# Performance work log

Measured on AMD Instinct MI355X. Metric: run time of the kernel, lower is better.

## Reference

```python
import jax, jax.numpy as jnp
import numpy as np

B, S, D, H = 2, 2048, 1024, 16
HD = D // H


def setup_inputs() -> dict:
    key = jax.random.key(0)
    ks = jax.random.split(key, 9)
    x = jax.random.normal(ks[0], (B, S, D), dtype=jnp.float32)
    scale = 1.0 / np.sqrt(D)
    Wq = jax.random.normal(ks[1], (D, D), dtype=jnp.float32) * scale
    bq = jnp.zeros((D,), dtype=jnp.float32)
    Wk = jax.random.normal(ks[2], (D, D), dtype=jnp.float32) * scale
    bk = jnp.zeros((D,), dtype=jnp.float32)
    Wv = jax.random.normal(ks[3], (D, D), dtype=jnp.float32) * scale
    bv = jnp.zeros((D,), dtype=jnp.float32)
    Wo = jax.random.normal(ks[4], (D, D), dtype=jnp.float32) * scale
    bo = jnp.zeros((D,), dtype=jnp.float32)
    return {"x": x, "Wq": Wq, "bq": bq, "Wk": Wk, "bk": bk,
            "Wv": Wv, "bv": bv, "Wo": Wo, "bo": bo}


def reference(x, Wq, bq, Wk, bk, Wv, bv, Wo, bo):
    b, s, d = x.shape
    h, hd = H, HD
    # torch Linear: y = x @ W.T + b
    q = (x @ Wq.T + bq).reshape(b, s, h, hd).transpose(0, 2, 1, 3)  # (b,h,s,hd)
    k = (x @ Wk.T + bk).reshape(b, s, h, hd).transpose(0, 2, 1, 3)
    v = (x @ Wv.T + bv).reshape(b, s, h, hd).transpose(0, 2, 1, 3)
    scores = jnp.einsum('bhqd,bhkd->bhqk', q, k) / np.sqrt(hd)  # (b,h,s,s)
    # FAITHFUL to source: softmax over dim=1 (head axis), not the key axis.
    attn = jax.nn.softmax(scores, axis=1)
    # dropout is identity at inference
    out = jnp.einsum('bhqk,bhkd->bhqd', attn, v)  # (b,h,s,hd)
    out = out.transpose(0, 2, 1, 3).reshape(b, s, d)
    return out @ Wo.T + bo
```

## Files before the change

kernel.cpp:

```cpp
#include <hip/hip_runtime.h>
#include <hip/hip_bf16.h>
#include <cstdint>
#include <cstddef>


typedef __bf16 bf16x8 __attribute__((ext_vector_type(8)));
typedef __bf16 bf16x4 __attribute__((ext_vector_type(4)));
typedef float floatx4 __attribute__((ext_vector_type(4)));

#define S_LEN 2048
#define DIM 1024
#define NH 16
#define HD 64
#define MTOT 4096

__global__ void cast_f32_bf16(const float* __restrict__ s, __bf16* __restrict__ d, int n) {
    int i = (blockIdx.x * blockDim.x + threadIdx.x) * 4;
    if (i < n) {
        float4 v = *(const float4*)&s[i];
        bf16x4 o;
        o.x = (__bf16)v.x; o.y = (__bf16)v.y; o.z = (__bf16)v.z; o.w = (__bf16)v.w;
        *(bf16x4*)&d[i] = o;
    }
}

template <typename OUT_T>
__global__ __launch_bounds__(256, 2) void gemm_bt(const __bf16* __restrict__ A,
                                                  const __bf16* __restrict__ Bw,
                                                  const float* __restrict__ bias,
                                                  OUT_T* __restrict__ C,
                                                  int M, int N, int K) {
    const int tm = blockIdx.y * 128;
    const int tn = blockIdx.x * 128;
    __shared__ __bf16 As[128 * 40];
    __shared__ __bf16 Bs[128 * 40];
    const int tid = threadIdx.x;
    const int wid = tid >> 6, lane = tid & 63;
    const int wm = (wid >> 1) * 64, wn = (wid & 1) * 64;
    const int l15 = lane & 15, quad = lane >> 4;
    floatx4 acc[4][4] = {};
    for (int k0 = 0; k0 < K; k0 += 32) {
        __syncthreads();
#pragma unroll
        for (int i = 0; i < 2; ++i) {
            int c = i * 256 + tid;
            int row = c >> 2, kc = (c & 3) * 8;
            *(bf16x8*)&As[row * 40 + kc] = *(const bf16x8*)&A[(size_t)(tm + row) * K + k0 + kc];
            *(bf16x8*)&Bs[row * 40 + kc] = *(const bf16x8*)&Bw[(size_t)(tn + row) * K + k0 + kc];
        }
        __syncthreads();
        bf16x8 af[4], bf[4];
#pragma unroll
        for (int t = 0; t < 4; ++t) {
            af[t] = *(const bf16x8*)&As[(wm + t * 16 + l15) * 40 + quad * 8];
            bf[t] = *(const bf16x8*)&Bs[(wn + t * 16 + l15) * 40 + quad * 8];
        }
#pragma unroll
        for (int im = 0; im < 4; ++im)
#pragma unroll
            for (int in = 0; in < 4; ++in)
                acc[im][in] = __builtin_amdgcn_mfma_f32_16x16x32_bf16(af[im], bf[in], acc[im][in], 0, 0, 0);
    }
#pragma unroll
    for (int im = 0; im < 4; ++im)
#pragma unroll
        for (int in = 0; in < 4; ++in)
#pragma unroll
            for (int r = 0; r < 4; ++r) {
                int row = tm + wm + im * 16 + quad * 4 + r;
                int col = tn + wn + in * 16 + l15;
                float v = acc[im][in][r] + bias[col];
                C[(size_t)row * N + col] = (OUT_T)v;
            }
}

__global__ void transpose_bf16(const __bf16* __restrict__ src, __bf16* __restrict__ dst,
                               int M, int N) {
    __shared__ __bf16 t[32][33];
    int bx = blockIdx.x * 32;
    int by = blockIdx.y * 32;
    int x = threadIdx.x, y = threadIdx.y;
#pragma unroll
    for (int i = 0; i < 32; i += 8) t[y + i][x] = src[(size_t)(by + y + i) * N + bx + x];
    __syncthreads();
#pragma unroll
    for (int i = 0; i < 32; i += 8) dst[(size_t)(bx + y + i) * M + by + x] = t[x][y + i];
}

__global__ __launch_bounds__(256, 2) void den_kernel(const __bf16* __restrict__ Q,
                                                     const __bf16* __restrict__ Km,
                                                     __bf16* __restrict__ rd) {
    const int b = blockIdx.z, qt = blockIdx.y * 128, kt = blockIdx.x * 128;
    __shared__ __bf16 Qs[128 * 72];
    __shared__ __bf16 Ks[128 * 72];
    const int tid = threadIdx.x;
    const int wid = tid >> 6, lane = tid & 63;
    const int wm = (wid >> 1) * 64, wn = (wid & 1) * 64;
    const int l15 = lane & 15, quad = lane >> 4;
    float den[4][4][4] = {};
    const size_t qbase = ((size_t)b * S_LEN + qt) * DIM;
    const size_t kbase = ((size_t)b * S_LEN + kt) * DIM;
    for (int h = 0; h < NH; ++h) {
        __syncthreads();
#pragma unroll
        for (int i = 0; i < 4; ++i) {
            int c = i * 256 + tid;
            int row = c >> 3, kc = (c & 7) * 8;
            *(bf16x8*)&Qs[row * 72 + kc] = *(const bf16x8*)&Q[qbase + (size_t)row * DIM + h * HD + kc];
            *(bf16x8*)&Ks[row * 72 + kc] = *(const bf16x8*)&Km[kbase + (size_t)row * DIM + h * HD + kc];
        }
        __syncthreads();
        floatx4 acc[4][4] = {};
#pragma unroll
        for (int kc = 0; kc < 2; ++kc) {
            bf16x8 af[4], bf[4];
#pragma unroll
            for (int t = 0; t < 4; ++t) {
                af[t] = *(const bf16x8*)&Qs[(wm + t * 16 + l15) * 72 + kc * 32 + quad * 8];
                bf[t] = *(const bf16x8*)&Ks[(wn + t * 16 + l15) * 72 + kc * 32 + quad * 8];
            }
#pragma unroll
            for (int im = 0; im < 4; ++im)
#pragma unroll
                for (int in = 0; in < 4; ++in)
                    acc[im][in] = __builtin_amdgcn_mfma_f32_16x16x32_bf16(af[im], bf[in], acc[im][in], 0, 0, 0);
        }
#pragma unroll
        for (int im = 0; im < 4; ++im)
#pragma unroll
            for (int in = 0; in < 4; ++in)
#pragma unroll
                for (int r = 0; r < 4; ++r)
                    den[im][in][r] += __expf(acc[im][in][r] * 0.125f);
    }
#pragma unroll
    for (int im = 0; im < 4; ++im)
#pragma unroll
        for (int in = 0; in < 4; ++in)
#pragma unroll
            for (int r = 0; r < 4; ++r) {
                int row = qt + wm + im * 16 + quad * 4 + r;
                int col = kt + wn + in * 16 + l15;
                rd[((size_t)b * S_LEN + row) * S_LEN + col] = (__bf16)(1.0f / den[im][in][r]);
            }
}

__global__ __launch_bounds__(256, 2) void attn_kernel(const __bf16* __restrict__ Q,
                                                      const __bf16* __restrict__ Km,
                                                      const __bf16* __restrict__ Vt,
                                                      const __bf16* __restrict__ rd,
                                                      __bf16* __restrict__ AO) {
    const int qt = blockIdx.x * 128, h = blockIdx.y, b = blockIdx.z;
    __shared__ __bf16 KV[128 * 72];
    __shared__ __bf16 Ps[128 * 136];
    const int tid = threadIdx.x;
    const int wid = tid >> 6, lane = tid & 63;
    const int wm = (wid >> 1) * 64, wn = (wid & 1) * 64;
    const int l15 = lane & 15, quad = lane >> 4;
    const size_t qrow0 = (size_t)b * S_LEN + qt;
    bf16x8 qf[4][2];
#pragma unroll
    for (int im = 0; im < 4; ++im)
#pragma unroll
        for (int kc = 0; kc < 2; ++kc)
            qf[im][kc] = *(const bf16x8*)&Q[(qrow0 + wm + im * 16 + l15) * DIM + h * HD + kc * 32 + quad * 8];
    floatx4 oacc[2][4] = {};
    const size_t kbase = ((size_t)b * S_LEN) * DIM;
    for (int kt = 0; kt < S_LEN; kt += 128) {
        __syncthreads();
#pragma unroll
        for (int i = 0; i < 4; ++i) {
            int c = i * 256 + tid;
            int row = c >> 3, kc = (c & 7) * 8;
            *(bf16x8*)&KV[row * 72 + kc] = *(const bf16x8*)&Km[kbase + (size_t)(kt + row) * DIM + h * HD + kc];
        }
#pragma unroll
        for (int i = 0; i < 8; ++i) {
            int c = i * 256 + tid;
            int row = c >> 4, cc = (c & 15) * 8;
            *(bf16x8*)&Ps[row * 136 + cc] =
                *(const bf16x8*)&rd[((size_t)b * S_LEN + qt + row) * S_LEN + kt + cc];
        }
        __syncthreads();
        floatx4 acc[4][4] = {};
#pragma unroll
        for (int kc = 0; kc < 2; ++kc) {
            bf16x8 bfr[4];
#pragma unroll
            for (int t = 0; t < 4; ++t)
                bfr[t] = *(const bf16x8*)&KV[(wn + t * 16 + l15) * 72 + kc * 32 + quad * 8];
#pragma unroll
            for (int im = 0; im < 4; ++im)
#pragma unroll
                for (int in = 0; in < 4; ++in)
                    acc[im][in] = __builtin_amdgcn_mfma_f32_16x16x32_bf16(qf[im][kc], bfr[in], acc[im][in], 0, 0, 0);
        }
#pragma unroll
        for (int im = 0; im < 4; ++im)
#pragma unroll
            for (int in = 0; in < 4; ++in)
#pragma unroll
                for (int r = 0; r < 4; ++r) {
                    int row = wm + im * 16 + quad * 4 + r;
                    int col = wn + in * 16 + l15;
                    float rdv = (float)Ps[row * 136 + col];
                    float p = __expf(acc[im][in][r] * 0.125f) * rdv;
                    Ps[row * 136 + col] = (__bf16)p;
                }
        __syncthreads();
#pragma unroll
        for (int i = 0; i < 4; ++i) {
            int c = i * 256 + tid;
            int row = c >> 4, cc = (c & 15) * 8;
            *(bf16x8*)&KV[row * 136 + cc] =
                *(const bf16x8*)&Vt[((size_t)h * HD + row) * MTOT + b * S_LEN + kt + cc];
        }
        __syncthreads();
        const int qr = wid * 32;
#pragma unroll
        for (int kc = 0; kc < 4; ++kc) {
            bf16x8 pa[2], vb[4];
#pragma unroll
            for (int t = 0; t < 2; ++t)
                pa[t] = *(const bf16x8*)&Ps[(qr + t * 16 + l15) * 136 + kc * 32 + quad * 8];
#pragma unroll
            for (int t = 0; t < 4; ++t)
                vb[t] = *(const bf16x8*)&KV[(t * 16 + l15) * 136 + kc * 32 + quad * 8];
#pragma unroll
            for (int im = 0; im < 2; ++im)
#pragma unroll
                for (int n = 0; n < 4; ++n)
                    oacc[im][n] = __builtin_amdgcn_mfma_f32_16x16x32_bf16(pa[im], vb[n], oacc[im][n], 0, 0, 0);
        }
    }
    const int qr = wid * 32;
#pragma unroll
    for (int im = 0; im < 2; ++im)
#pragma unroll
        for (int n = 0; n < 4; ++n)
#pragma unroll
            for (int r = 0; r < 4; ++r) {
                int row = qt + qr + im * 16 + quad * 4 + r;
                int col = h * HD + n * 16 + l15;
                AO[((size_t)b * S_LEN + row) * DIM + col] = (__bf16)(oacc[im][n][r]);
            }
}

extern "C" void kernel_launch(void* const* d_in, const int* in_sizes, int n_in,
                              void* d_out, int out_size, void* d_ws, size_t ws_size,
                              hipStream_t stream) {
    const float* x  = (const float*)d_in[0];
    const float* Wq = (const float*)d_in[1];
    const float* bq = (const float*)d_in[2];
    const float* Wk = (const float*)d_in[3];
    const float* bk = (const float*)d_in[4];
    const float* Wv = (const float*)d_in[5];
    const float* bv = (const float*)d_in[6];
    const float* Wo = (const float*)d_in[7];
    const float* bo = (const float*)d_in[8];
    float* out = (float*)d_out;

    char* ws = (char*)d_ws;
    const size_t MB = 1u << 20;
    __bf16* xb  = (__bf16*)(ws);
    __bf16* Wqb = (__bf16*)(ws + 8 * MB);
    __bf16* Wkb = (__bf16*)(ws + 10 * MB);
    __bf16* Wvb = (__bf16*)(ws + 12 * MB);
    __bf16* Wob = (__bf16*)(ws + 14 * MB);
    __bf16* Qb  = (__bf16*)(ws + 16 * MB);
    __bf16* Kb  = (__bf16*)(ws + 24 * MB);
    __bf16* Vb  = (__bf16*)(ws + 32 * MB);
    __bf16* Vtb = (__bf16*)(ws + 40 * MB);
    __bf16* rd  = (__bf16*)(ws + 48 * MB);
    __bf16* AOb = (__bf16*)(ws + 64 * MB);

    cast_f32_bf16<<<4096, 256, 0, stream>>>(x,  xb,  MTOT * DIM);
    cast_f32_bf16<<<1024, 256, 0, stream>>>(Wq, Wqb, DIM * DIM);
    cast_f32_bf16<<<1024, 256, 0, stream>>>(Wk, Wkb, DIM * DIM);
    cast_f32_bf16<<<1024, 256, 0, stream>>>(Wv, Wvb, DIM * DIM);
    cast_f32_bf16<<<1024, 256, 0, stream>>>(Wo, Wob, DIM * DIM);

    dim3 gproj(DIM / 128, MTOT / 128);
    gemm_bt<__bf16><<<gproj, 256, 0, stream>>>(xb, Wqb, bq, Qb, MTOT, DIM, DIM);
    gemm_bt<__bf16><<<gproj, 256, 0, stream>>>(xb, Wkb, bk, Kb, MTOT, DIM, DIM);
    gemm_bt<__bf16><<<gproj, 256, 0, stream>>>(xb, Wvb, bv, Vb, MTOT, DIM, DIM);

    dim3 gtr(DIM / 32, MTOT / 32);
    transpose_bf16<<<gtr, dim3(32, 8), 0, stream>>>(Vb, Vtb, MTOT, DIM);

    dim3 gden(S_LEN / 128, S_LEN / 128, 2);
    den_kernel<<<gden, 256, 0, stream>>>(Qb, Kb, rd);

    dim3 gattn(S_LEN / 128, NH, 2);
    attn_kernel<<<gattn, 256, 0, stream>>>(Qb, Kb, Vtb, rd, AOb);

    gemm_bt<float><<<gproj, 256, 0, stream>>>(AOb, Wob, bo, out, MTOT, DIM, DIM);
}
```

Before: 317.1 us.

## Rewrite GEMM, denominator and attention kernels with direct global-to-LDS loads

```diff
diff --git a/kernel.cpp b/kernel.cpp
--- a/kernel.cpp
+++ b/kernel.cpp
@@ -6,6 +6,8 @@
 
 typedef __bf16 bf16x8 __attribute__((ext_vector_type(8)));
 typedef __bf16 bf16x4 __attribute__((ext_vector_type(4)));
+typedef _Float16 f16x4 __attribute__((ext_vector_type(4)));
+typedef _Float16 f16x8 __attribute__((ext_vector_type(8)));
 typedef float floatx4 __attribute__((ext_vector_type(4)));
 
 #define S_LEN 2048
@@ -13,6 +15,12 @@
 #define NH 16
 #define HD 64
 #define MTOT 4096
+
+__device__ __forceinline__ void g2l16(const void* g, void* l) {
+    __builtin_amdgcn_global_load_lds(
+        (const __attribute__((address_space(1))) void*)g,
+        (__attribute__((address_space(3))) void*)l, 16, 0, 0);
+}
 
 __global__ void cast_f32_bf16(const float* __restrict__ s, __bf16* __restrict__ d, int n) {
     int i = (blockIdx.x * blockDim.x + threadIdx.x) * 4;
@@ -25,60 +33,65 @@
 }
 
 template <typename OUT_T>
-__global__ __launch_bounds__(256, 2) void gemm_bt(const __bf16* __restrict__ A,
-                                                  const __bf16* __restrict__ Bw,
-                                                  const float* __restrict__ bias,
-                                                  OUT_T* __restrict__ C,
-                                                  int M, int N, int K) {
-    const int tm = blockIdx.y * 128;
-    const int tn = blockIdx.x * 128;
-    __shared__ __bf16 As[128 * 40];
-    __shared__ __bf16 Bs[128 * 40];
-    const int tid = threadIdx.x;
-    const int wid = tid >> 6, lane = tid & 63;
-    const int wm = (wid >> 1) * 64, wn = (wid & 1) * 64;
+__global__ __launch_bounds__(256, 2) void gemm_bt2(const __bf16* __restrict__ A,
+                                                   const __bf16* __restrict__ Bw,
+                                                   const float* __restrict__ bias,
+                                                   OUT_T* __restrict__ C,
+                                                   int M, int N, int K) {
+    const int tm = blockIdx.y * 128, tn = blockIdx.x * 64;
+    __shared__ __bf16 As[2 * 128 * 32];
+    __shared__ __bf16 Bs[2 * 64 * 32];
+    const int tid = threadIdx.x, wid = tid >> 6, lane = tid & 63;
     const int l15 = lane & 15, quad = lane >> 4;
-    floatx4 acc[4][4] = {};
-    for (int k0 = 0; k0 < K; k0 += 32) {
-        __syncthreads();
+    const int wm = (wid >> 1) * 64, wn = (wid & 1) * 32;
+    floatx4 acc[4][2] = {};
+    for (int k0 = 0; k0 < K; k0 += 64) {
+        __syncthreads();
+#pragma unroll
+        for (int i = 0; i < 4; ++i) {
+            int slot = i * 256 + tid;
+            int p = slot >> 9, r = (slot >> 2) & 127, c8 = (slot & 3) * 8;
+            g2l16(&A[(size_t)(tm + r) * K + k0 + p * 32 + c8], &As[slot * 8]);
+        }
 #pragma unroll
         for (int i = 0; i < 2; ++i) {
-            int c = i * 256 + tid;
-            int row = c >> 2, kc = (c & 3) * 8;
-            *(bf16x8*)&As[row * 40 + kc] = *(const bf16x8*)&A[(size_t)(tm + row) * K + k0 + kc];
-            *(bf16x8*)&Bs[row * 40 + kc] = *(const bf16x8*)&Bw[(size_t)(tn + row) * K + k0 + kc];
-        }
-        __syncthreads();
-        bf16x8 af[4], bf[4];
-#pragma unroll
-        for (int t = 0; t < 4; ++t) {
-            af[t] = *(const bf16x8*)&As[(wm + t * 16 + l15) * 40 + quad * 8];
-            bf[t] = *(const bf16x8*)&Bs[(wn + t * 16 + l15) * 40 + quad * 8];
-        }
-#pragma unroll
-        for (int im = 0; im < 4; ++im)
-#pragma unroll
-            for (int in = 0; in < 4; ++in)
-                acc[im][in] = __builtin_amdgcn_mfma_f32_16x16x32_bf16(af[im], bf[in], acc[im][in], 0, 0, 0);
+            int slot = i * 256 + tid;
+            int p = slot >> 8, r = (slot >> 2) & 63, c8 = (slot & 3) * 8;
+            g2l16(&Bw[(size_t)(tn + r) * K + k0 + p * 32 + c8], &Bs[slot * 8]);
+        }
+        __syncthreads();
+#pragma unroll
+        for (int kc = 0; kc < 2; ++kc) {
+            bf16x8 af[4], bf[2];
+#pragma unroll
+            for (int t = 0; t < 4; ++t)
+                af[t] = *(const bf16x8*)&As[kc * 4096 + (wm + t * 16 + l15) * 32 + quad * 8];
+#pragma unroll
+            for (int t = 0; t < 2; ++t)
+                bf[t] = *(const bf16x8*)&Bs[kc * 2048 + (wn + t * 16 + l15) * 32 + quad * 8];
+#pragma unroll
+            for (int im = 0; im < 4; ++im)
+#pragma unroll
+                for (int in = 0; in < 2; ++in)
+                    acc[im][in] = __builtin_amdgcn_mfma_f32_16x16x32_bf16(af[im], bf[in], acc[im][in], 0, 0, 0);
+        }
     }
 #pragma unroll
     for (int im = 0; im < 4; ++im)
 #pragma unroll
-        for (int in = 0; in < 4; ++in)
+        for (int in = 0; in < 2; ++in)
 #pragma unroll
             for (int r = 0; r < 4; ++r) {
                 int row = tm + wm + im * 16 + quad * 4 + r;
                 int col = tn + wn + in * 16 + l15;
-                float v = acc[im][in][r] + bias[col];
-                C[(size_t)row * N + col] = (OUT_T)v;
-            }
-}
-
-__global__ void transpose_bf16(const __bf16* __restrict__ src, __bf16* __restrict__ dst,
-                               int M, int N) {
-    __shared__ __bf16 t[32][33];
-    int bx = blockIdx.x * 32;
-    int by = blockIdx.y * 32;
+                C[(size_t)row * N + col] = (OUT_T)(acc[im][in][r] + bias[col]);
+            }
+}
+
+__global__ void transpose16(const ushort* __restrict__ src, ushort* __restrict__ dst,
+                            int M, int N) {
+    __shared__ ushort t[32][33];
+    int bx = blockIdx.x * 32, by = blockIdx.y * 32;
     int x = threadIdx.x, y = threadIdx.y;
 #pragma unroll
     for (int i = 0; i < 32; i += 8) t[y + i][x] = src[(size_t)(by + y + i) * N + bx + x];
@@ -87,162 +100,131 @@
     for (int i = 0; i < 32; i += 8) dst[(size_t)(bx + y + i) * M + by + x] = t[x][y + i];
 }
 
-__global__ __launch_bounds__(256, 2) void den_kernel(const __bf16* __restrict__ Q,
-                                                     const __bf16* __restrict__ Km,
-                                                     __bf16* __restrict__ rd) {
-    const int b = blockIdx.z, qt = blockIdx.y * 128, kt = blockIdx.x * 128;
-    __shared__ __bf16 Qs[128 * 72];
-    __shared__ __bf16 Ks[128 * 72];
-    const int tid = threadIdx.x;
-    const int wid = tid >> 6, lane = tid & 63;
-    const int wm = (wid >> 1) * 64, wn = (wid & 1) * 64;
+__global__ __launch_bounds__(256, 4) void den2(const __bf16* __restrict__ Q,
+                                               const __bf16* __restrict__ Km,
+                                               __bf16* __restrict__ rd) {
+    const int kt = blockIdx.x * 128, qt = blockIdx.y * 64, b = blockIdx.z;
+    __shared__ __bf16 Qs[2 * 64 * 32];
+    __shared__ __bf16 Ks[2 * 128 * 32];
+    const int tid = threadIdx.x, wid = tid >> 6, lane = tid & 63;
     const int l15 = lane & 15, quad = lane >> 4;
-    float den[4][4][4] = {};
-    const size_t qbase = ((size_t)b * S_LEN + qt) * DIM;
-    const size_t kbase = ((size_t)b * S_LEN + kt) * DIM;
+    const int wq = wid * 16;
+    floatx4 dsum[8] = {};
     for (int h = 0; h < NH; ++h) {
         __syncthreads();
 #pragma unroll
-        for (int i = 0; i < 4; ++i) {
-            int c = i * 256 + tid;
-            int row = c >> 3, kc = (c & 7) * 8;
-            *(bf16x8*)&Qs[row * 72 + kc] = *(const bf16x8*)&Q[qbase + (size_t)row * DIM + h * HD + kc];
-            *(bf16x8*)&Ks[row * 72 + kc] = *(const bf16x8*)&Km[kbase + (size_t)row * DIM + h * HD + kc];
-        }
-        __syncthreads();
-        floatx4 acc[4][4] = {};
-#pragma unroll
-        for (int kc = 0; kc < 2; ++kc) {
-            bf16x8 af[4], bf[4];
-#pragma unroll
-            for (int t = 0; t < 4; ++t) {
-                af[t] = *(const bf16x8*)&Qs[(wm + t * 16 + l15) * 72 + kc * 32 + quad * 8];
-                bf[t] = *(const bf16x8*)&Ks[(wn + t * 16 + l15) * 72 + kc * 32 + quad * 8];
-            }
-#pragma unroll
-            for (int im = 0; im < 4; ++im)
-#pragma unroll
-                for (int in = 0; in < 4; ++in)
-                    acc[im][in] = __builtin_amdgcn_mfma_f32_16x16x32_bf16(af[im], bf[in], acc[im][in], 0, 0, 0);
-        }
-#pragma unroll
-        for (int im = 0; im < 4; ++im)
-#pragma unroll
-            for (int in = 0; in < 4; ++in)
-#pragma unroll
-                for (int r = 0; r < 4; ++r)
-                    den[im][in][r] += __expf(acc[im][in][r] * 0.125f);
-    }
-#pragma unroll
-    for (int im = 0; im < 4; ++im)
-#pragma unroll
-        for (int in = 0; in < 4; ++in)
+        for (int i = 0; i < 2; ++i) {
+            int slot = i * 256 + tid;
+            int p = slot >> 8, r = (slot >> 2) & 63, c8 = (slot & 3) * 8;
+            g2l16(&Q[(size_t)(b * S_LEN + qt + r) * DIM + h * HD + p * 32 + c8], &Qs[slot * 8]);
+        }
+#pragma unroll
+        for (int i = 0; i < 4; ++i) {
+            int slot = i * 256 + tid;
+            int p = slot >> 9, r = (slot >> 2) & 127, c8 = (slot & 3) * 8;
+            g2l16(&Km[(size_t)(b * S_LEN + kt + r) * DIM + h * HD + p * 32 + c8], &Ks[slot * 8]);
+        }
+        __syncthreads();
+        bf16x8 af0 = *(const bf16x8*)&Qs[(wq + l15) * 32 + quad * 8];
+        bf16x8 af1 = *(const bf16x8*)&Qs[2048 + (wq + l15) * 32 + quad * 8];
+#pragma unroll
+        for (int n = 0; n < 8; ++n) {
+            bf16x8 b0 = *(const bf16x8*)&Ks[(n * 16 + l15) * 32 + quad * 8];
+            bf16x8 b1 = *(const bf16x8*)&Ks[4096 + (n * 16 + l15) * 32 + quad * 8];
+            floatx4 acc = {};
+            acc = __builtin_amdgcn_mfma_f32_16x16x32_bf16(af0, b0, acc, 0, 0, 0);
+            acc = __builtin_amdgcn_mfma_f32_16x16x32_bf16(af1, b1, acc, 0, 0, 0);
+#pragma unroll
+            for (int r = 0; r < 4; ++r) dsum[n][r] += __expf(acc[r] * 0.125f);
+        }
+    }
+#pragma unroll
+    for (int n = 0; n < 8; ++n)
+#pragma unroll
+        for (int r = 0; r < 4; ++r) {
+            int q = qt + wq + quad * 4 + r;
+            int k = kt + n * 16 + l15;
+            rd[(size_t)(b * S_LEN + q) * S_LEN + k] = (__bf16)(1.0f / dsum[n][r]);
+        }
+}
+
+__global__ __launch_bounds__(256, 2) void attn2(const __bf16* __restrict__ Q,
+                                                const __bf16* __restrict__ Km,
+                                                const _Float16* __restrict__ Vt,
+                                                const __bf16* __restrict__ rd,
+                                                __bf16* __restrict__ AO) {
+    const int qt = blockIdx.x * 128, h = blockIdx.y, b = blockIdx.z;
+    __shared__ __bf16 Ks[2 * 128 * 32];
+    __shared__ __bf16 rds[128 * 136];
+    __shared__ _Float16 Vts[64 * 136];
+    const int tid = threadIdx.x, wid = tid >> 6, lane = tid & 63;
+    const int l15 = lane & 15, quad = lane >> 4;
+    const int wq = wid * 32;
+    bf16x8 qf[2][2];
+#pragma unroll
+    for (int np = 0; np < 2; ++np)
+#pragma unroll
+        for (int kc = 0; kc < 2; ++kc)
+            qf[np][kc] = *(const bf16x8*)&Q[(size_t)(b * S_LEN + qt + wq + np * 16 + l15) * DIM +
+                                            h * HD + kc * 32 + quad * 8];
+    floatx4 oacc[2][4] = {};
+    for (int kt = 0; kt < S_LEN; kt += 128) {
+        __syncthreads();
+#pragma unroll
+        for (int i = 0; i < 4; ++i) {
+            int slot = i * 256 + tid;
+            int p = slot >> 9, r = (slot >> 2) & 127, c8 = (slot & 3) * 8;
+            g2l16(&Km[(size_t)(b * S_LEN + kt + r) * DIM + h * HD + p * 32 + c8], &Ks[slot * 8]);
+        }
+#pragma unroll
+        for (int i = 0; i < 8; ++i) {
+            int slot = i * 256 + tid;
+            int r = slot >> 4, c = (slot & 15) * 8;
+            *(bf16x8*)&rds[r * 136 + c] =
+                *(const bf16x8*)&rd[(size_t)(b * S_LEN + qt + r) * S_LEN + kt + c];
+        }
+#pragma unroll
+        for (int i = 0; i < 4; ++i) {
+            int slot = i * 256 + tid;
+            int r = slot >> 4, c = (slot & 15) * 8;
+            *(f16x8*)&Vts[r * 136 + c] =
+                *(const f16x8*)&Vt[(size_t)(h * HD + r) * MTOT + b * S_LEN + kt + c];
+        }
+        __syncthreads();
+#pragma unroll
+        for (int mp = 0; mp < 8; ++mp) {
+            bf16x8 kf0 = *(const bf16x8*)&Ks[(mp * 16 + l15) * 32 + quad * 8];
+            bf16x8 kf1 = *(const bf16x8*)&Ks[4096 + (mp * 16 + l15) * 32 + quad * 8];
+            floatx4 s0 = {}, s1 = {};
+            s0 = __builtin_amdgcn_mfma_f32_16x16x32_bf16(kf0, qf[0][0], s0, 0, 0, 0);
+            s0 = __builtin_amdgcn_mfma_f32_16x16x32_bf16(kf1, qf[0][1], s0, 0, 0, 0);
+            s1 = __builtin_amdgcn_mfma_f32_16x16x32_bf16(kf0, qf[1][0], s1, 0, 0, 0);
+            s1 = __builtin_amdgcn_mfma_f32_16x16x32_bf16(kf1, qf[1][1], s1, 0, 0, 0);
+            bf16x4 rv0 = *(const bf16x4*)&rds[(wq + l15) * 136 + mp * 16 + quad * 4];
+            bf16x4 rv1 = *(const bf16x4*)&rds[(wq + 16 + l15) * 136 + mp * 16 + quad * 4];
+            f16x4 pa0, pa1;
 #pragma unroll
             for (int r = 0; r < 4; ++r) {
-                int row = qt + wm + im * 16 + quad * 4 + r;
-                int col = kt + wn + in * 16 + l15;
-                rd[((size_t)b * S_LEN + row) * S_LEN + col] = (__bf16)(1.0f / den[im][in][r]);
-            }
-}
-
-__global__ __launch_bounds__(256, 2) void attn_kernel(const __bf16* __restrict__ Q,
-                                                      const __bf16* __restrict__ Km,
-                                                      const __bf16* __restrict__ Vt,
-                                                      const __bf16* __restrict__ rd,
-                                                      __bf16* __restrict__ AO) {
-    const int qt = blockIdx.x * 128, h = blockIdx.y, b = blockIdx.z;
-    __shared__ __bf16 KV[128 * 72];
-    __shared__ __bf16 Ps[128 * 136];
-    const int tid = threadIdx.x;
-    const int wid = tid >> 6, lane = tid & 63;
-    const int wm = (wid >> 1) * 64, wn = (wid & 1) * 64;
-    const int l15 = lane & 15, quad = lane >> 4;
-    const size_t qrow0 = (size_t)b * S_LEN + qt;
-    bf16x8 qf[4][2];
-#pragma unroll
-    for (int im = 0; im < 4; ++im)
-#pragma unroll
-        for (int kc = 0; kc < 2; ++kc)
-            qf[im][kc] = *(const bf16x8*)&Q[(qrow0 + wm + im * 16 + l15) * DIM + h * HD + kc * 32 + quad * 8];
-    floatx4 oacc[2][4] = {};
-    const size_t kbase = ((size_t)b * S_LEN) * DIM;
-    for (int kt = 0; kt < S_LEN; kt += 128) {
-        __syncthreads();
-#pragma unroll
-        for (int i = 0; i < 4; ++i) {
-            int c = i * 256 + tid;
-            int row = c >> 3, kc = (c & 7) * 8;
-            *(bf16x8*)&KV[row * 72 + kc] = *(const bf16x8*)&Km[kbase + (size_t)(kt + row) * DIM + h * HD + kc];
-        }
-#pragma unroll
-        for (int i = 0; i < 8; ++i) {
-            int c = i * 256 + tid;
-            int row = c >> 4, cc = (c & 15) * 8;
-            *(bf16x8*)&Ps[row * 136 + cc] =
-                *(const bf16x8*)&rd[((size_t)b * S_LEN + qt + row) * S_LEN + kt + cc];
-        }
-        __syncthreads();
-        floatx4 acc[4][4] = {};
-#pragma unroll
-        for (int kc = 0; kc < 2; ++kc) {
-            bf16x8 bfr[4];
-#pragma unroll
-            for (int t = 0; t < 4; ++t)
-                bfr[t] = *(const bf16x8*)&KV[(wn + t * 16 + l15) * 72 + kc * 32 + quad * 8];
-#pragma unroll
-            for (int im = 0; im < 4; ++im)
-#pragma unroll
-                for (int in = 0; in < 4; ++in)
-                    acc[im][in] = __builtin_amdgcn_mfma_f32_16x16x32_bf16(qf[im][kc], bfr[in], acc[im][in], 0, 0, 0);
-        }
-#pragma unroll
-        for (int im = 0; im < 4; ++im)
-#pragma unroll
-            for (int in = 0; in < 4; ++in)
-#pragma unroll
-                for (int r = 0; r < 4; ++r) {
-                    int row = wm + im * 16 + quad * 4 + r;
-                    int col = wn + in * 16 + l15;
-                    float rdv = (float)Ps[row * 136 + col];
-                    float p = __expf(acc[im][in][r] * 0.125f) * rdv;
-                    Ps[row * 136 + col] = (__bf16)p;
-                }
-        __syncthreads();
-#pragma unroll
-        for (int i = 0; i < 4; ++i) {
-            int c = i * 256 + tid;
-            int row = c >> 4, cc = (c & 15) * 8;
-            *(bf16x8*)&KV[row * 136 + cc] =
-                *(const bf16x8*)&Vt[((size_t)h * HD + row) * MTOT + b * S_LEN + kt + cc];
-        }
-        __syncthreads();
-        const int qr = wid * 32;
-#pragma unroll
-        for (int kc = 0; kc < 4; ++kc) {
-            bf16x8 pa[2], vb[4];
-#pragma unroll
-            for (int t = 0; t < 2; ++t)
-                pa[t] = *(const bf16x8*)&Ps[(qr + t * 16 + l15) * 136 + kc * 32 + quad * 8];
-#pragma unroll
-            for (int t = 0; t < 4; ++t)
-                vb[t] = *(const bf16x8*)&KV[(t * 16 + l15) * 136 + kc * 32 + quad * 8];
-#pragma unroll
-            for (int im = 0; im < 2; ++im)
-#pragma unroll
-                for (int n = 0; n < 4; ++n)
-                    oacc[im][n] = __builtin_amdgcn_mfma_f32_16x16x32_bf16(pa[im], vb[n], oacc[im][n], 0, 0, 0);
-        }
-    }
-    const int qr = wid * 32;
-#pragma unroll
-    for (int im = 0; im < 2; ++im)
+                pa0[r] = (_Float16)(__expf(s0[r] * 0.125f) * (float)rv0[r]);
+                pa1[r] = (_Float16)(__expf(s1[r] * 0.125f) * (float)rv1[r]);
+            }
+#pragma unroll
+            for (int n = 0; n < 4; ++n) {
+                f16x4 vb = *(const f16x4*)&Vts[(n * 16 + l15) * 136 + mp * 16 + quad * 4];
+                oacc[0][n] = __builtin_amdgcn_mfma_f32_16x16x16f16(pa0, vb, oacc[0][n], 0, 0, 0);
+                oacc[1][n] = __builtin_amdgcn_mfma_f32_16x16x16f16(pa1, vb, oacc[1][n], 0, 0, 0);
+            }
+        }
+    }
+#pragma unroll
+    for (int np = 0; np < 2; ++np)
 #pragma unroll
         for (int n = 0; n < 4; ++n)
 #pragma unroll
             for (int r = 0; r < 4; ++r) {
-                int row = qt + qr + im * 16 + quad * 4 + r;
+                int row = qt + wq + np * 16 + quad * 4 + r;
                 int col = h * HD + n * 16 + l15;
-                AO[((size_t)b * S_LEN + row) * DIM + col] = (__bf16)(oacc[im][n][r]);
+                AO[(size_t)(b * S_LEN + row) * DIM + col] = (__bf16)oacc[np][n][r];
             }
 }
 
@@ -262,17 +244,17 @@
 
     char* ws = (char*)d_ws;
     const size_t MB = 1u << 20;
-    __bf16* xb  = (__bf16*)(ws);
-    __bf16* Wqb = (__bf16*)(ws + 8 * MB);
-    __bf16* Wkb = (__bf16*)(ws + 10 * MB);
-    __bf16* Wvb = (__bf16*)(ws + 12 * MB);
-    __bf16* Wob = (__bf16*)(ws + 14 * MB);
-    __bf16* Qb  = (__bf16*)(ws + 16 * MB);
-    __bf16* Kb  = (__bf16*)(ws + 24 * MB);
-    __bf16* Vb  = (__bf16*)(ws + 32 * MB);
-    __bf16* Vtb = (__bf16*)(ws + 40 * MB);
-    __bf16* rd  = (__bf16*)(ws + 48 * MB);
-    __bf16* AOb = (__bf16*)(ws + 64 * MB);
+    __bf16*    xb  = (__bf16*)(ws);
+    __bf16*    Wqb = (__bf16*)(ws + 8 * MB);
+    __bf16*    Wkb = (__bf16*)(ws + 10 * MB);
+    __bf16*    Wvb = (__bf16*)(ws + 12 * MB);
+    __bf16*    Wob = (__bf16*)(ws + 14 * MB);
+    __bf16*    Qb  = (__bf16*)(ws + 16 * MB);
+    __bf16*    Kb  = (__bf16*)(ws + 24 * MB);
+    _Float16*  Vh  = (_Float16*)(ws + 32 * MB);
+    _Float16*  VtH = (_Float16*)(ws + 40 * MB);
+    __bf16*    rd  = (__bf16*)(ws + 48 * MB);
+    __bf16*    AOb = (__bf16*)(ws + 64 * MB);
 
     cast_f32_bf16<<<4096, 256, 0, stream>>>(x,  xb,  MTOT * DIM);
     cast_f32_bf16<<<1024, 256, 0, stream>>>(Wq, Wqb, DIM * DIM);
@@ -280,19 +262,19 @@
     cast_f32_bf16<<<1024, 256, 0, stream>>>(Wv, Wvb, DIM * DIM);
     cast_f32_bf16<<<1024, 256, 0, stream>>>(Wo, Wob, DIM * DIM);
 
-    dim3 gproj(DIM / 128, MTOT / 128);
-    gemm_bt<__bf16><<<gproj, 256, 0, stream>>>(xb, Wqb, bq, Qb, MTOT, DIM, DIM);
-    gemm_bt<__bf16><<<gproj, 256, 0, stream>>>(xb, Wkb, bk, Kb, MTOT, DIM, DIM);
-    gemm_bt<__bf16><<<gproj, 256, 0, stream>>>(xb, Wvb, bv, Vb, MTOT, DIM, DIM);
+    dim3 gproj(DIM / 64, MTOT / 128);
+    gemm_bt2<__bf16><<<gproj, 256, 0, stream>>>(xb, Wqb, bq, Qb, MTOT, DIM, DIM);
+    gemm_bt2<__bf16><<<gproj, 256, 0, stream>>>(xb, Wkb, bk, Kb, MTOT, DIM, DIM);
+    gemm_bt2<_Float16><<<gproj, 256, 0, stream>>>(xb, Wvb, bv, Vh, MTOT, DIM, DIM);
 
     dim3 gtr(DIM / 32, MTOT / 32);
-    transpose_bf16<<<gtr, dim3(32, 8), 0, stream>>>(Vb, Vtb, MTOT, DIM);
-
-    dim3 gden(S_LEN / 128, S_LEN / 128, 2);
-    den_kernel<<<gden, 256, 0, stream>>>(Qb, Kb, rd);
+    transpose16<<<gtr, dim3(32, 8), 0, stream>>>((const ushort*)Vh, (ushort*)VtH, MTOT, DIM);
+
+    dim3 gden(S_LEN / 128, S_LEN / 64, 2);
+    den2<<<gden, 256, 0, stream>>>(Qb, Kb, rd);
 
     dim3 gattn(S_LEN / 128, NH, 2);
-    attn_kernel<<<gattn, 256, 0, stream>>>(Qb, Kb, Vtb, rd, AOb);
-
-    gemm_bt<float><<<gproj, 256, 0, stream>>>(AOb, Wob, bo, out, MTOT, DIM, DIM);
-}
+    attn2<<<gattn, 256, 0, stream>>>(Qb, Kb, VtH, rd, AOb);
+
+    gemm_bt2<float><<<gproj, 256, 0, stream>>>(AOb, Wob, bo, out, MTOT, DIM, DIM);
+}
```

New measurement: 310.7 us. 2.0% less time.
